# Kernel optimization log

Measured on AMD Instinct MI355X. Metric: run time of the kernel, lower is better.

The kernel has to match this reference:

```python
import jax, jax.numpy as jnp
import numpy as np


def setup_inputs() -> dict:
    key = jax.random.key(0)
    k1, k2 = jax.random.split(key)
    B, C, H, W = 1, 128, 96, 128
    feat_l = jax.random.normal(k1, (B, C, H, W), dtype=jnp.float32)
    feat_r = jax.random.normal(k2, (B, C, H, W), dtype=jnp.float32)
    return {"feat_l": feat_l, "feat_r": feat_r, "scale_x": 4, "scale_y": 4}


def reference(feat_l, feat_r, scale_x, scale_y):
    B, C, H, W = feat_l.shape
    _, _, H_R, W_R = feat_r.shape
    # Full correlation volume: [B, H, W, H_R*W_R]  (the huge intermediate)
    corr = jnp.einsum('bchw,bcij->bhwij', feat_l, feat_r).reshape(B, H, W, H_R * W_R)
    flow_cost = jnp.max(corr, axis=3)           # [B, H, W]
    flat_idx = jnp.argmax(corr, axis=3)         # [B, H, W] int
    # Decode argmax index -> flow (u, v) relative to pixel grid
    xoff = jnp.arange(W)                        # [W]
    yoff = jnp.arange(H)                        # [H]
    u = -((flat_idx % W_R) * scale_x - xoff[None, None, :]).astype(jnp.float32)
    v = -((flat_idx // W_R) * scale_y - yoff[None, :, None]).astype(jnp.float32)
    flow = jnp.stack([u, v], axis=3)            # [B, H, W, 2]
    return flow, flow_cost
```

## Files before the change

kernel.cpp:

```cpp
#include <hip/hip_runtime.h>

#define K_TOT 128
#define H_DIM 96
#define W_DIM 128
#define M_TOT (H_DIM * W_DIM)
#define N_TOT (H_DIM * W_DIM)
#define SCALE 4
#define NEG_INF (-3.402823e38f)

#define KP 384
#define NCH 12

typedef _Float16 f16x8 __attribute__((ext_vector_type(8)));
typedef float f32x16 __attribute__((ext_vector_type(16)));

#define ASYNC16(lds_ptr, g_ptr) \
  __builtin_amdgcn_global_load_lds( \
      (const __attribute__((address_space(1))) unsigned int*)(g_ptr), \
      (__attribute__((address_space(3))) unsigned int*)(lds_ptr), 16, 0, 0)

__global__ __launch_bounds__(256)
void split_prep_kernel(const float* __restrict__ L, const float* __restrict__ R,
                       _Float16* __restrict__ Ls, _Float16* __restrict__ Rs,
                       unsigned long long* __restrict__ keys) {
    const int t = threadIdx.x;
    if (blockIdx.x >= 384) {
        int m = (blockIdx.x - 384) * 256 + t;
        if (m < M_TOT) keys[m] = 0ull;
        return;
    }
    __shared__ __align__(16) _Float16 T[3][64][136];
    const int isR = blockIdx.x >= 192;
    const int P0 = (blockIdx.x - (isR ? 192 : 0)) * 64;
    const float* src = isR ? R : L;
    _Float16* dst = isR ? Rs : Ls;

    const int p4 = (t & 15) * 4;
    const int k0 = t >> 4;
#pragma unroll
    for (int it = 0; it < 8; ++it) {
        const int k = k0 + it * 16;
        float4 v = *(const float4*)&src[(size_t)k * M_TOT + P0 + p4];
        float xs[4] = {v.x, v.y, v.z, v.w};
#pragma unroll
        for (int j = 0; j < 4; ++j) {
            _Float16 h = (_Float16)xs[j];
            float hf = (float)h;
            float r = xs[j] - hf;
            T[0][p4 + j][k] = h;
            T[1][p4 + j][k] = (_Float16)(r * 64.0f);
            T[2][p4 + j][k] = (_Float16)(hf * 0.015625f);
        }
    }
    __syncthreads();
#pragma unroll
    for (int it = 0; it < 12; ++it) {
        const int cid = it * 256 + t;
        const int row = cid / 48;
        const int seg = cid % 48;
        const int sec = seg >> 4;
        const int sub = seg & 15;
        const int plane = (sec == 0) ? 0 : (isR ? sec : 3 - sec);
        float4 v = *(const float4*)&T[plane][row][sub * 8];
        *(float4*)&dst[(size_t)(P0 + row) * KP + seg * 8] = v;
    }
}

__global__ __launch_bounds__(256, 4)
void mfma_corr_kernel(const _Float16* __restrict__ Ls, const _Float16* __restrict__ Rs,
                      unsigned long long* __restrict__ keys) {
    __shared__ __align__(16) char smem[32768];

    const int tid  = threadIdx.x;
    const int lane = tid & 63;
    const int wid  = tid >> 6;
    const int wr   = wid >> 1;
    const int wc   = wid & 1;
    const int bid  = blockIdx.x;
    const int idx  = (bid & 7) * 1152 + (bid >> 3);
    const int mt   = idx / 96;
    const int nt   = idx % 96;
    const int m0   = mt * 128;
    const int n0   = nt * 128;

    f32x16 acc[2][2];
#pragma unroll
    for (int mi = 0; mi < 2; ++mi)
#pragma unroll
        for (int ni = 0; ni < 2; ++ni) acc[mi][ni] = (f32x16)(0.0f);

    const int lr4  = lane >> 2;
    const int lsl  = lane & 3;
    const int col  = lane & 31;
    const int hi   = lane >> 5;

    auto stage = [&](int buf, int ch) {
#pragma unroll
        for (int i = 0; i < 4; ++i) {
            const int s  = wid * 4 + i;
            const int rl = (s & 7) * 16 + lr4;
            const int ko = lsl ^ ((rl >> 1) & 3);
            if (s < 8) {
                ASYNC16(smem + buf * 8192 + s * 1024,
                        Ls + (size_t)(m0 + rl) * KP + ch * 32 + ko * 8);
            } else {
                ASYNC16(smem + 16384 + buf * 8192 + (s - 8) * 1024,
                        Rs + (size_t)(n0 + rl) * KP + ch * 32 + ko * 8);
            }
        }
    };

    stage(0, 0);
    __syncthreads();
    int cur = 0;
    for (int ch = 0; ch < NCH; ++ch) {
        if (ch + 1 < NCH) stage(cur ^ 1, ch + 1);
#pragma unroll
        for (int kk = 0; kk < 2; ++kk) {
            f16x8 a[2], b[2];
#pragma unroll
            for (int mi = 0; mi < 2; ++mi) {
                const int rl = wr * 64 + mi * 32 + col;
                const int sl = (kk * 2 + hi) ^ ((rl >> 1) & 3);
                a[mi] = *(const f16x8*)(smem + cur * 8192 + rl * 64 + sl * 16);
            }
#pragma unroll
            for (int ni = 0; ni < 2; ++ni) {
                const int rl = wc * 64 + ni * 32 + col;
                const int sl = (kk * 2 + hi) ^ ((rl >> 1) & 3);
                b[ni] = *(const f16x8*)(smem + 16384 + cur * 8192 + rl * 64 + sl * 16);
            }
#pragma unroll
            for (int mi = 0; mi < 2; ++mi)
#pragma unroll
                for (int ni = 0; ni < 2; ++ni)
                    acc[mi][ni] = __builtin_amdgcn_mfma_f32_32x32x16_f16(
                        a[mi], b[ni], acc[mi][ni], 0, 0, 0);
        }
        __syncthreads();
        cur ^= 1;
    }

    float* vals = (float*)smem;
    int*   idxs = (int*)(smem + 8704);
#pragma unroll
    for (int mi = 0; mi < 2; ++mi) {
#pragma unroll
        for (int reg = 0; reg < 16; ++reg) {
            float best = acc[mi][0][reg];
            int bni = 0;
            if (acc[mi][1][reg] > best) { best = acc[mi][1][reg]; bni = 1; }
            int n = n0 + wc * 64 + bni * 32 + col;
#pragma unroll
            for (int d = 16; d >= 8; d >>= 1) {
                float ov = __shfl_xor(best, d, 64);
                int   oi = __shfl_xor(n, d, 64);
                if (ov > best || (ov == best && oi < n)) { best = ov; n = oi; }
            }
            if ((lane & 24) == 0) {
                const int row = wr * 64 + mi * 32 + (reg & 3) + 8 * (reg >> 2) + 4 * hi;
                const int c   = wc * 8 + (lane & 7);
                vals[row * 17 + c] = best;
                idxs[row * 17 + c] = n;
            }
        }
    }
    __syncthreads();
    if (tid < 128) {
        float bv = vals[tid * 17 + 0]; int bi = idxs[tid * 17 + 0];
#pragma unroll
        for (int c = 1; c < 16; ++c) {
            float v = vals[tid * 17 + c]; int ix = idxs[tid * 17 + c];
            if (v > bv || (v == bv && ix < bi)) { bv = v; bi = ix; }
        }
        unsigned vb = __float_as_uint(bv);
        vb = (vb & 0x80000000u) ? ~vb : (vb | 0x80000000u);
        unsigned long long key = ((unsigned long long)vb << 32) | (unsigned)(~bi);
        atomicMax(&keys[m0 + tid], key);
    }
}

__global__ void finalize_keys_kernel(const unsigned long long* __restrict__ keys,
                                     float* __restrict__ out) {
    int m = blockIdx.x * blockDim.x + threadIdx.x;
    if (m >= M_TOT) return;
    unsigned long long key = keys[m];
    unsigned hi = (unsigned)(key >> 32);
    unsigned bits = (hi & 0x80000000u) ? (hi & 0x7fffffffu) : ~hi;
    float v = __uint_as_float(bits);
    int idx = (int)(~(unsigned)(key & 0xffffffffu));
    int h = m / W_DIM, w = m % W_DIM;
    int i = idx / W_DIM, j = idx % W_DIM;
    out[m * 2 + 0] = (float)(w - SCALE * j);
    out[m * 2 + 1] = (float)(h - SCALE * i);
    out[2 * M_TOT + m] = v;
}

#define BM 128
#define BN 128
#define KB 32
__global__ __launch_bounds__(256)
void corr_argmax_kernel(const float* __restrict__ L, const float* __restrict__ R,
                        float* __restrict__ pbest, int* __restrict__ pidx,
                        int nsplit) {
    __shared__ float As[KB][BM];
    __shared__ float Bs[KB][BN];
    const int tid = threadIdx.x;
    const int mtiles = M_TOT / BM;
    const int mt = blockIdx.x % mtiles;
    const int s  = blockIdx.x / mtiles;
    const int m0 = mt * BM;
    const int ns = N_TOT / nsplit;
    const int ntiles = ns / BN;
    const int tx = tid & 15;
    const int ty = tid >> 4;
    float rbest[8]; int ridx[8];
#pragma unroll
    for (int i = 0; i < 8; ++i) { rbest[i] = NEG_INF; ridx[i] = 0; }
    for (int nt = 0; nt < ntiles; ++nt) {
        const int n0 = s * ns + nt * BN;
        float acc[8][8];
#pragma unroll
        for (int i = 0; i < 8; ++i)
#pragma unroll
            for (int j = 0; j < 8; ++j) acc[i][j] = 0.f;
        for (int kb = 0; kb < K_TOT; kb += KB) {
            __syncthreads();
#pragma unroll
            for (int r = 0; r < 4; ++r) {
                int f  = tid + 256 * r;
                int kk = f >> 5;
                int c4 = f & 31;
                float4 va = *reinterpret_cast<const float4*>(&L[(size_t)(kb + kk) * M_TOT + m0 + c4 * 4]);
                *reinterpret_cast<float4*>(&As[kk][c4 * 4]) = va;
                float4 vb = *reinterpret_cast<const float4*>(&R[(size_t)(kb + kk) * N_TOT + n0 + c4 * 4]);
                *reinterpret_cast<float4*>(&Bs[kk][c4 * 4]) = vb;
            }
            __syncthreads();
#pragma unroll 4
            for (int kk = 0; kk < KB; ++kk) {
                float4 a0 = *reinterpret_cast<const float4*>(&As[kk][ty * 4]);
                float4 a1 = *reinterpret_cast<const float4*>(&As[kk][64 + ty * 4]);
                float4 b0 = *reinterpret_cast<const float4*>(&Bs[kk][tx * 4]);
                float4 b1 = *reinterpret_cast<const float4*>(&Bs[kk][64 + tx * 4]);
                float a[8] = {a0.x, a0.y, a0.z, a0.w, a1.x, a1.y, a1.z, a1.w};
                float b[8] = {b0.x, b0.y, b0.z, b0.w, b1.x, b1.y, b1.z, b1.w};
#pragma unroll
                for (int i = 0; i < 8; ++i)
#pragma unroll
                    for (int j = 0; j < 8; ++j)
                        acc[i][j] = fmaf(a[i], b[j], acc[i][j]);
            }
        }
#pragma unroll
        for (int i = 0; i < 8; ++i)
#pragma unroll
            for (int jh = 0; jh < 2; ++jh)
#pragma unroll
                for (int jj = 0; jj < 4; ++jj) {
                    int n = n0 + jh * 64 + tx * 4 + jj;
                    float v = acc[i][jh * 4 + jj];
                    if (v > rbest[i]) { rbest[i] = v; ridx[i] = n; }
                }
    }
    __syncthreads();
    float (*redv)[BM] = reinterpret_cast<float(*)[BM]>(&As[0][0]);
    int   (*redi)[BM] = reinterpret_cast<int  (*)[BM]>(&Bs[0][0]);
#pragma unroll
    for (int i = 0; i < 8; ++i) {
        int row = (i >> 2) * 64 + ty * 4 + (i & 3);
        redv[tx][row] = rbest[i];
        redi[tx][row] = ridx[i];
    }
    __syncthreads();
    if (tid < BM) {
        float bv = NEG_INF; int bi = 0x7fffffff;
        for (int t = 0; t < 16; ++t) {
            float v  = redv[t][tid];
            int   ix = redi[t][tid];
            if (v > bv || (v == bv && ix < bi)) { bv = v; bi = ix; }
        }
        pbest[(size_t)s * M_TOT + m0 + tid] = bv;
        pidx [(size_t)s * M_TOT + m0 + tid] = bi;
    }
}

__global__ void finalize_parts_kernel(const float* __restrict__ pbest,
                                      const int* __restrict__ pidx,
                                      float* __restrict__ out, int nsplit) {
    int m = blockIdx.x * blockDim.x + threadIdx.x;
    if (m >= M_TOT) return;
    float bv = NEG_INF; int bi = 0x7fffffff;
    for (int s = 0; s < nsplit; ++s) {
        float v  = pbest[(size_t)s * M_TOT + m];
        int   ix = pidx [(size_t)s * M_TOT + m];
        if (v > bv || (v == bv && ix < bi)) { bv = v; bi = ix; }
    }
    int h = m / W_DIM, w = m % W_DIM;
    int i = bi / W_DIM, j = bi % W_DIM;
    out[m * 2 + 0] = (float)(w - SCALE * j);
    out[m * 2 + 1] = (float)(h - SCALE * i);
    out[2 * M_TOT + m] = bv;
}

extern "C" void kernel_launch(void* const* d_in, const int* in_sizes, int n_in,
                              void* d_out, int out_size, void* d_ws, size_t ws_size,
                              hipStream_t stream) {
    const float* L = (const float*)d_in[0];
    const float* R = (const float*)d_in[1];
    float* out = (float*)d_out;

    const size_t PKbytes = (size_t)M_TOT * KP * sizeof(_Float16);
    const size_t need = 2 * PKbytes + (size_t)M_TOT * 8;
    if (ws_size >= need) {
        _Float16* Ls = (_Float16*)d_ws;
        _Float16* Rs = (_Float16*)((char*)d_ws + PKbytes);
        unsigned long long* keys = (unsigned long long*)((char*)d_ws + 2 * PKbytes);
        split_prep_kernel<<<dim3(432), dim3(256), 0, stream>>>(L, R, Ls, Rs, keys);
        mfma_corr_kernel<<<dim3((M_TOT / 128) * (N_TOT / 128)), dim3(256), 0, stream>>>(Ls, Rs, keys);
        finalize_keys_kernel<<<dim3(48), dim3(256), 0, stream>>>(keys, out);
    } else {
        int nsplit = 8;
        while (nsplit > 1 && (size_t)nsplit * M_TOT * 8 > ws_size) nsplit >>= 1;
        float* pbest = (float*)d_ws;
        int*   pidx  = (int*)((char*)d_ws + (size_t)nsplit * M_TOT * sizeof(float));
        corr_argmax_kernel<<<dim3((M_TOT / BM) * nsplit), dim3(256), 0, stream>>>(L, R, pbest, pidx, nsplit);
        finalize_parts_kernel<<<dim3((M_TOT + 255) / 256), dim3(256), 0, stream>>>(pbest, pidx, out, nsplit);
    }
}
```

Baseline: 271.6 us.

## Pre-swizzle operands into MFMA fragment order and load directly to registers

The prep kernel now writes the fp16 split operands in a per-64-row slab layout that matches the MFMA 32x32x16 fragment order, so each lane's 16-byte fragment sits at a contiguous offset. The correlation kernel drops the LDS double-buffered async staging and its barriers, and instead loads fragments straight from global memory into registers with a three-deep software prefetch. The block-to-tile mapping changes so each XCD works on a fixed set of N tiles, and launch bounds drop to 3 waves per SIMD to make room for the extra fragment registers. The cost is that operands are no longer shared across waves through LDS, so global/L2 traffic per block goes up, and register pressure and occupancy change.

Result: faster. 259.2 us (-4.6%).

```diff
diff --git a/kernel.cpp b/kernel.cpp
--- a/kernel.cpp
+++ b/kernel.cpp
@@ -9,15 +9,11 @@
 #define NEG_INF (-3.402823e38f)
 
 #define KP 384
-#define NCH 12
+#define NH 24
+#define SLAB_F16 24576
 
 typedef _Float16 f16x8 __attribute__((ext_vector_type(8)));
 typedef float f32x16 __attribute__((ext_vector_type(16)));
-
-#define ASYNC16(lds_ptr, g_ptr) \
-  __builtin_amdgcn_global_load_lds( \
-      (const __attribute__((address_space(1))) unsigned int*)(g_ptr), \
-      (__attribute__((address_space(3))) unsigned int*)(lds_ptr), 16, 0, 0)
 
 __global__ __launch_bounds__(256)
 void split_prep_kernel(const float* __restrict__ L, const float* __restrict__ R,
@@ -29,9 +25,10 @@
         if (m < M_TOT) keys[m] = 0ull;
         return;
     }
-    __shared__ __align__(16) _Float16 T[3][64][136];
-    const int isR = blockIdx.x >= 192;
-    const int P0 = (blockIdx.x - (isR ? 192 : 0)) * 64;
+    __shared__ __align__(16) _Float16 T[3][64][144];
+    const int isR  = blockIdx.x >= 192;
+    const int slab = blockIdx.x - (isR ? 192 : 0);
+    const int P0   = slab * 64;
     const float* src = isR ? R : L;
     _Float16* dst = isR ? Rs : Ls;
 
@@ -55,94 +52,70 @@
     __syncthreads();
 #pragma unroll
     for (int it = 0; it < 12; ++it) {
-        const int cid = it * 256 + t;
-        const int row = cid / 48;
-        const int seg = cid % 48;
-        const int sec = seg >> 4;
-        const int sub = seg & 15;
+        const int c    = it * 256 + t;
+        const int col  = c & 31;
+        const int hi   = (c >> 5) & 1;
+        const int op   = (c >> 6) & 1;
+        const int half = c >> 7;
+        const int sec  = half >> 3;
+        const int kb   = (half & 7) * 16 + hi * 8;
         const int plane = (sec == 0) ? 0 : (isR ? sec : 3 - sec);
-        float4 v = *(const float4*)&T[plane][row][sub * 8];
-        *(float4*)&dst[(size_t)(P0 + row) * KP + seg * 8] = v;
-    }
-}
-
-__global__ __launch_bounds__(256, 4)
+        const int row  = op * 32 + col;
+        float4 v = *(const float4*)&T[plane][row][kb];
+        *(float4*)&dst[(size_t)slab * SLAB_F16 + (size_t)c * 8] = v;
+    }
+}
+
+__global__ __launch_bounds__(256, 3)
 void mfma_corr_kernel(const _Float16* __restrict__ Ls, const _Float16* __restrict__ Rs,
                       unsigned long long* __restrict__ keys) {
-    __shared__ __align__(16) char smem[32768];
+    __shared__ float vals[128 * 17];
+    __shared__ int   idxs[128 * 17];
 
     const int tid  = threadIdx.x;
     const int lane = tid & 63;
     const int wid  = tid >> 6;
     const int wr   = wid >> 1;
     const int wc   = wid & 1;
+    const int col  = lane & 31;
+    const int hi   = lane >> 5;
     const int bid  = blockIdx.x;
-    const int idx  = (bid & 7) * 1152 + (bid >> 3);
-    const int mt   = idx / 96;
-    const int nt   = idx % 96;
+    const int xcd  = bid & 7;
+    const int b    = bid >> 3;
+    const int mt   = b / 12;
+    const int nt   = xcd * 12 + b % 12;
     const int m0   = mt * 128;
     const int n0   = nt * 128;
 
+    const _Float16* pA = Ls + (size_t)(mt * 2 + wr) * SLAB_F16 + lane * 8;
+    const _Float16* pB = Rs + (size_t)(nt * 2 + wc) * SLAB_F16 + lane * 8;
+
     f32x16 acc[2][2];
 #pragma unroll
     for (int mi = 0; mi < 2; ++mi)
 #pragma unroll
         for (int ni = 0; ni < 2; ++ni) acc[mi][ni] = (f32x16)(0.0f);
 
-    const int lr4  = lane >> 2;
-    const int lsl  = lane & 3;
-    const int col  = lane & 31;
-    const int hi   = lane >> 5;
-
-    auto stage = [&](int buf, int ch) {
-#pragma unroll
-        for (int i = 0; i < 4; ++i) {
-            const int s  = wid * 4 + i;
-            const int rl = (s & 7) * 16 + lr4;
-            const int ko = lsl ^ ((rl >> 1) & 3);
-            if (s < 8) {
-                ASYNC16(smem + buf * 8192 + s * 1024,
-                        Ls + (size_t)(m0 + rl) * KP + ch * 32 + ko * 8);
-            } else {
-                ASYNC16(smem + 16384 + buf * 8192 + (s - 8) * 1024,
-                        Rs + (size_t)(n0 + rl) * KP + ch * 32 + ko * 8);
-            }
-        }
-    };
-
-    stage(0, 0);
-    __syncthreads();
-    int cur = 0;
-    for (int ch = 0; ch < NCH; ++ch) {
-        if (ch + 1 < NCH) stage(cur ^ 1, ch + 1);
-#pragma unroll
-        for (int kk = 0; kk < 2; ++kk) {
-            f16x8 a[2], b[2];
-#pragma unroll
-            for (int mi = 0; mi < 2; ++mi) {
-                const int rl = wr * 64 + mi * 32 + col;
-                const int sl = (kk * 2 + hi) ^ ((rl >> 1) & 3);
-                a[mi] = *(const f16x8*)(smem + cur * 8192 + rl * 64 + sl * 16);
-            }
-#pragma unroll
-            for (int ni = 0; ni < 2; ++ni) {
-                const int rl = wc * 64 + ni * 32 + col;
-                const int sl = (kk * 2 + hi) ^ ((rl >> 1) & 3);
-                b[ni] = *(const f16x8*)(smem + 16384 + cur * 8192 + rl * 64 + sl * 16);
-            }
-#pragma unroll
-            for (int mi = 0; mi < 2; ++mi)
-#pragma unroll
-                for (int ni = 0; ni < 2; ++ni)
-                    acc[mi][ni] = __builtin_amdgcn_mfma_f32_32x32x16_f16(
-                        a[mi], b[ni], acc[mi][ni], 0, 0, 0);
-        }
-        __syncthreads();
-        cur ^= 1;
-    }
-
-    float* vals = (float*)smem;
-    int*   idxs = (int*)(smem + 8704);
+    f16x8 fA[3][2], fB[3][2];
+#define LOADH(hh, s) {                                              \
+        fA[s][0] = *(const f16x8*)(pA + (hh) * 1024);               \
+        fA[s][1] = *(const f16x8*)(pA + (hh) * 1024 + 512);         \
+        fB[s][0] = *(const f16x8*)(pB + (hh) * 1024);               \
+        fB[s][1] = *(const f16x8*)(pB + (hh) * 1024 + 512);         \
+    }
+    LOADH(0, 0);
+    LOADH(1, 1);
+#pragma unroll
+    for (int h = 0; h < NH; ++h) {
+        if (h + 2 < NH) LOADH(h + 2, (h + 2) % 3);
+        const int s = h % 3;
+        acc[0][0] = __builtin_amdgcn_mfma_f32_32x32x16_f16(fA[s][0], fB[s][0], acc[0][0], 0, 0, 0);
+        acc[0][1] = __builtin_amdgcn_mfma_f32_32x32x16_f16(fA[s][0], fB[s][1], acc[0][1], 0, 0, 0);
+        acc[1][0] = __builtin_amdgcn_mfma_f32_32x32x16_f16(fA[s][1], fB[s][0], acc[1][0], 0, 0, 0);
+        acc[1][1] = __builtin_amdgcn_mfma_f32_32x32x16_f16(fA[s][1], fB[s][1], acc[1][1], 0, 0, 0);
+    }
+#undef LOADH
+
 #pragma unroll
     for (int mi = 0; mi < 2; ++mi) {
 #pragma unroll
```
